# Performance work log

Hardware: AMD Instinct MI355X
Metric: run time of the kernel (lower is better)

The kernel has to match this reference:

```python
import jax, jax.numpy as jnp
import numpy as np

REALSHAPE = (32, 256, 256)   # even dims required
SHAPE = (32, 256, 129)       # rfft half-spectrum shape
MIDS = (16, 128, 128)
KCUT = 4
B, C = 4, 3


def _hs_np(f):
    # numpy mirror of Fourier.hermitian_symmetric (used only to build the constant feed mask)
    m0, m1, m2 = MIDS
    f = f.copy()
    f[m0+1:, 0, 0] = f[1:m0, 0, 0][::-1].conj()
    f[m0+1:, 0, m2] = f[1:m0, 0, m2][::-1].conj()
    f[m0+1:, m1, 0] = f[1:m0, m1, 0][::-1].conj()
    f[m0+1:, m1, m2] = f[1:m0, m1, m2][::-1].conj()
    f[0, m1+1:, 0] = f[0, 1:m1, 0][::-1].conj()
    f[0, m1+1:, m2] = f[0, 1:m1, m2][::-1].conj()
    f[m0, m1+1:, 0] = f[m0, 1:m1, 0][::-1].conj()
    f[m0, m1+1:, m2] = f[m0, 1:m1, m2][::-1].conj()
    f[m0+1:, m1+1:, 0] = f[1:m0, 1:m1, 0][::-1, ::-1].conj()
    f[m0+1:, 1:m1, 0] = f[1:m0, m1+1:, 0][::-1, ::-1].conj()
    f[m0+1:, m1+1:, m2] = f[1:m0, 1:m1, m2][::-1, ::-1].conj()
    f[m0+1:, 1:m1, m2] = f[1:m0, m1+1:, m2][::-1, ::-1].conj()
    return f


def _constants():
    ks = [np.fft.fftfreq(d, 1.0 / d) for d in SHAPE[:-1]] + [np.arange(SHAPE[-1])]
    kgrid = np.array(np.meshgrid(*ks, indexing='ij'))
    ksq = np.sum(kgrid ** 2, axis=0)
    holders = np.stack(np.meshgrid(*[np.arange(d) for d in SHAPE], indexing='ij'))
    same = np.all(np.stack([_hs_np(h) for h in holders]) == holders, axis=0)
    rem = same & (ksq <= KCUT ** 2)
    feed = np.stack([rem, rem.copy()])
    m0, m1, m2 = MIDS
    for idx in [(0, 0, 0), (0, 0, m2), (0, m1, 0), (0, m1, m2),
                (m0, 0, 0), (m0, 0, m2), (m0, m1, 0), (m0, m1, m2)]:
        feed[(1,) + idx] = False  # purely real corner modes
    feed_idx = np.nonzero(feed.reshape(-1))[0].astype(np.int32)
    ks_sel = np.stack([ksq, ksq])[feed]  # dimscale = (1,1,1)
    Pk = (1.0 / (ks_sel + 1.0) * float(np.prod(REALSHAPE))).astype(np.float32)
    grid = np.stack(np.meshgrid(*[np.arange(d) for d in REALSHAPE], indexing='ij')).astype(np.float32)
    return feed_idx, Pk, grid


def setup_inputs() -> dict:
    feed_idx, Pk, grid = _constants()
    key = jax.random.key(0)
    k1, k2 = jax.random.split(key)
    fr = jax.random.normal(k1, (B, C) + REALSHAPE, jnp.float32)
    seeds = jax.random.normal(k2, (1, 3 * feed_idx.size), jnp.float32)
    return {
        'fr': fr,
        'seeds': seeds,
        'Pk': jnp.asarray(Pk),
        'defscale': jnp.ones(3, jnp.float32),  # defscale / dimscale
        'grid': jnp.asarray(grid),
        'feed_idx': jnp.asarray(feed_idx),
    }


def _hs(f):
    # jax hermitian-symmetrize the rfft half-spectrum (writes are non-overlapping with reads)
    m0, m1, m2 = MIDS
    fl = lambda a: jnp.flip(a, 0).conj()
    fl2 = lambda a: jnp.flip(a, (0, 1)).conj()
    f = f.at[m0+1:, 0, 0].set(fl(f[1:m0, 0, 0]))
    f = f.at[m0+1:, 0, m2].set(fl(f[1:m0, 0, m2]))
    f = f.at[m0+1:, m1, 0].set(fl(f[1:m0, m1, 0]))
    f = f.at[m0+1:, m1, m2].set(fl(f[1:m0, m1, m2]))
    f = f.at[0, m1+1:, 0].set(fl(f[0, 1:m1, 0]))
    f = f.at[0, m1+1:, m2].set(fl(f[0, 1:m1, m2]))
    f = f.at[m0, m1+1:, 0].set(fl(f[m0, 1:m1, 0]))
    f = f.at[m0, m1+1:, m2].set(fl(f[m0, 1:m1, m2]))
    f = f.at[m0+1:, m1+1:, 0].set(fl2(f[1:m0, 1:m1, 0]))
    f = f.at[m0+1:, 1:m1, 0].set(fl2(f[1:m0, m1+1:, 0]))
    f = f.at[m0+1:, m1+1:, m2].set(fl2(f[1:m0, 1:m1, m2]))
    f = f.at[m0+1:, 1:m1, m2].set(fl2(f[1:m0, m1+1:, m2]))
    return f


def _forward(fr, seeds, Pk, defscale, grid, feed_idx):
    fdim = feed_idx.shape[0]
    # scale sparse coefficients by the power spectrum
    x = seeds.reshape(3, fdim) * Pk[None, :] * defscale[:, None]
    # scatter into the (2, *SHAPE) re/im spectrum via flat indices
    nfull = 2 * int(np.prod(SHAPE))
    arr = jnp.zeros((3, nfull), jnp.float32).at[:, feed_idx].set(x).reshape(3, 2, *SHAPE)
    comp = (arr[:, 0] + 1j * arr[:, 1]).astype(jnp.complex64)
    comp = jax.vmap(_hs)(comp)
    disp = jnp.fft.irfftn(comp[None], s=REALSHAPE, axes=(2, 3, 4))  # (1,3,D,H,W) float32
    D, H, W = REALSHAPE
    norm = (jnp.asarray(REALSHAPE, jnp.float32) - 1.0)[None, :, None, None, None]
    moved = 2.0 * ((grid[None] - disp) / norm) - 1.0  # normalized coords in [-1,1]
    gz, gy, gx = moved[0, 0], moved[0, 1], moved[0, 2]  # torch grid channel order [2,1,0] -> (x=W, y=H, z=D)
    # grid_sample: bilinear, padding_mode='border' (clamp float coords), align_corners=True
    fz = jnp.clip((gz + 1.0) * 0.5 * (D - 1), 0.0, D - 1)
    fy = jnp.clip((gy + 1.0) * 0.5 * (H - 1), 0.0, H - 1)
    fx = jnp.clip((gx + 1.0) * 0.5 * (W - 1), 0.0, W - 1)
    z0 = jnp.floor(fz); y0 = jnp.floor(fy); x0 = jnp.floor(fx)
    wz = fz - z0; wy = fy - y0; wx = fx - x0  # (D,H,W), broadcast against (B,C,D,H,W)
    z0i = z0.astype(jnp.int32); z1i = jnp.minimum(z0i + 1, D - 1)
    y0i = y0.astype(jnp.int32); y1i = jnp.minimum(y0i + 1, H - 1)
    x0i = x0.astype(jnp.int32); x1i = jnp.minimum(x0i + 1, W - 1)
    g = lambda zi, yi, xi: fr[:, :, zi, yi, xi]  # gather -> (B,C,D,H,W)
    c00 = g(z0i, y0i, x0i) * (1 - wx) + g(z0i, y0i, x1i) * wx
    c01 = g(z0i, y1i, x0i) * (1 - wx) + g(z0i, y1i, x1i) * wx
    c10 = g(z1i, y0i, x0i) * (1 - wx) + g(z1i, y0i, x1i) * wx
    c11 = g(z1i, y1i, x0i) * (1 - wx) + g(z1i, y1i, x1i) * wx
    c0 = c00 * (1 - wy) + c01 * wy
    c1 = c10 * (1 - wy) + c11 * wy
    return c0 * (1 - wz) + c1 * wz


def reference(fr, seeds, Pk, defscale, grid, feed_idx):
    return _forward(fr, seeds, Pk, defscale, grid, feed_idx)
```

## Files before the change

### kernel.cpp

```cpp
#include <hip/hip_runtime.h>
#include <math.h>

#define D0 32
#define D1 256
#define D2 256
#define HS2 129
#define NVOX (D0*D1*D2)
#define KMAX 4
#define NK 9
#define NK2 5
#define NCH 3
#define BATCH 4
#define FCH 3
#define NBC (BATCH*FCH)
#define C_FLOATS (NCH*NK*NK*NK2*2)

typedef float v2f __attribute__((ext_vector_type(2)));

__global__ __launch_bounds__(256) void build_S(
    const float* __restrict__ seeds, const float* __restrict__ Pk,
    const float* __restrict__ defscale, const int* __restrict__ feed_idx,
    int fdim, float* __restrict__ S)
{
    __shared__ float C[C_FLOATS];
    __shared__ int fed[NK*NK];
    int t = threadIdx.x;
    for (int i = t; i < C_FLOATS; i += 256) C[i] = 0.0f;
    if (t < NK*NK) fed[t] = 0;
    __syncthreads();
    float ds0 = defscale[0], ds1 = defscale[1], ds2 = defscale[2];
    const int STR_RI = D0 * D1 * HS2;
    const int STR_A  = D1 * HS2;
    for (int j = t; j < fdim; j += 256) {
        int idx = feed_idx[j];
        int ri = idx / STR_RI; int r = idx - ri * STR_RI;
        int a  = r / STR_A;    r -= a * STR_A;
        int b  = r / HS2;      int c = r - b * HS2;
        int k0 = (a < D0/2) ? a : a - D0;
        int k1 = (b < D1/2) ? b : b - D1;
        if (k0 < -KMAX || k0 > KMAX || k1 < -KMAX || k1 > KMAX || c > KMAX) continue;
        int i0 = k0 + KMAX, i1 = k1 + KMAX;
        float pk = Pk[j];
        int base = ((i0*NK + i1)*NK2 + c)*2 + ri;
        C[base]                 = seeds[0*fdim + j] * pk * ds0;
        C[base + 1*NK*NK*NK2*2] = seeds[1*fdim + j] * pk * ds1;
        C[base + 2*NK*NK*NK2*2] = seeds[2*fdim + j] * pk * ds2;
        if (c == 0) fed[i0*NK + i1] = 1;
    }
    __syncthreads();
    if (t < NK*NK && !fed[t]) {
        int i0 = t / NK, i1 = t - i0*NK;
        int m0 = (NK-1) - i0, m1 = (NK-1) - i1;
        for (int ch = 0; ch < NCH; ++ch) {
            int dst = ((ch*NK*NK + i0*NK + i1)*NK2 + 0)*2;
            int src = ((ch*NK*NK + m0*NK + m1)*NK2 + 0)*2;
            C[dst]   = C[src];
            C[dst+1] = -C[src+1];
        }
    }
    __syncthreads();

    int zyl = t >> 3;
    int g   = t & 7;
    int zy = blockIdx.x * 32 + zyl;
    int z = zy >> 8, y = zy & 255;

    float w0r[NK], w0i[NK], w1r[NK], w1i[NK];
    {
        float th = (float)z * (6.28318530717958647692f / (float)D0);
        float sb, cb; __sincosf(th, &sb, &cb);
        w0r[KMAX] = 1.0f; w0i[KMAX] = 0.0f;
        float pr = 1.0f, pi = 0.0f;
        #pragma unroll
        for (int k = 1; k <= KMAX; ++k) {
            float nr = pr*cb - pi*sb, ni = pr*sb + pi*cb;
            pr = nr; pi = ni;
            w0r[KMAX+k] = pr; w0i[KMAX+k] = pi;
            w0r[KMAX-k] = pr; w0i[KMAX-k] = -pi;
        }
    }
    {
        float th = (float)y * (6.28318530717958647692f / (float)D1);
        float sb, cb; __sincosf(th, &sb, &cb);
        w1r[KMAX] = 1.0f; w1i[KMAX] = 0.0f;
        float pr = 1.0f, pi = 0.0f;
        #pragma unroll
        for (int k = 1; k <= KMAX; ++k) {
            float nr = pr*cb - pi*sb, ni = pr*sb + pi*cb;
            pr = nr; pi = ni;
            w1r[KMAX+k] = pr; w1i[KMAX+k] = pi;
            w1r[KMAX-k] = pr; w1i[KMAX-k] = -pi;
        }
    }

    float Sr[NCH*NK2], Si[NCH*NK2];
    #pragma unroll
    for (int i = 0; i < NCH*NK2; ++i) { Sr[i] = 0.0f; Si[i] = 0.0f; }

    for (int m = g; m < NK*NK; m += 8) {
        int i0 = m / NK, i1 = m - i0*NK;
        float Tr = w0r[i0]*w1r[i1] - w0i[i0]*w1i[i1];
        float Ti = w0r[i0]*w1i[i1] + w0i[i0]*w1r[i1];
        const float* Cp = C + m*NK2*2;
        #pragma unroll
        for (int ch = 0; ch < NCH; ++ch) {
            #pragma unroll
            for (int k2 = 0; k2 < NK2; ++k2) {
                float cr = Cp[ch*(NK*NK*NK2*2) + k2*2];
                float ci = Cp[ch*(NK*NK*NK2*2) + k2*2 + 1];
                int o = ch*NK2 + k2;
                Sr[o] += cr*Tr - ci*Ti;
                Si[o] += cr*Ti + ci*Tr;
            }
        }
    }

    #pragma unroll
    for (int off = 4; off >= 1; off >>= 1) {
        #pragma unroll
        for (int i = 0; i < NCH*NK2; ++i) {
            Sr[i] += __shfl_down(Sr[i], off, 8);
            Si[i] += __shfl_down(Si[i], off, 8);
        }
    }

    if (g == 0) {
        const float invN = 1.0f / (float)NVOX;
        float* Sp = S + (size_t)zy * 32;
        #pragma unroll
        for (int ch = 0; ch < NCH; ++ch) {
            #pragma unroll
            for (int k2 = 0; k2 < NK2; ++k2) {
                int o = ch*NK2 + k2;
                float sc = (k2 == 0) ? invN : 2.0f*invN;
                Sp[ch*10 + k2*2 + 0] = Sr[o] * sc;
                Sp[ch*10 + k2*2 + 1] = Si[o] * sc;
            }
        }
    }
}

__global__ __launch_bounds__(256) void deform_sample(
    const float* __restrict__ fr, const float* __restrict__ S,
    float* __restrict__ out)
{
    int i = blockIdx.x;
    int u = i & 7;
    int b  = u >> 1;
    int zh = u & 1;
    int j = i >> 3;
    int z = (zh << 4) + (j >> 8);
    int y = j & 255;
    int zy = (z << 8) + y;
    int x = threadIdx.x;

    const float* __restrict__ Sp = S + (size_t)zy * 32;
    float s[30];
    #pragma unroll
    for (int q = 0; q < 30; ++q) s[q] = Sp[q];

    float th = (float)x * (6.28318530717958647692f / (float)D2);
    float sb, cb; __sincosf(th, &sb, &cb);
    float ckr[KMAX], cks[KMAX];
    ckr[0] = cb; cks[0] = sb;
    #pragma unroll
    for (int k = 1; k < KMAX; ++k) {
        float nr = ckr[k-1]*cb - cks[k-1]*sb;
        float ni = cks[k-1]*cb + ckr[k-1]*sb;
        ckr[k] = nr; cks[k] = ni;
    }

    float d[NCH];
    #pragma unroll
    for (int ch = 0; ch < NCH; ++ch) {
        float acc = s[ch*10 + 0];
        #pragma unroll
        for (int k = 1; k <= KMAX; ++k)
            acc += s[ch*10 + k*2]*ckr[k-1] - s[ch*10 + k*2 + 1]*cks[k-1];
        d[ch] = acc;
    }

    float fz = fminf(fmaxf((float)z - d[0], 0.0f), (float)(D0-1));
    float fy = fminf(fmaxf((float)y - d[1], 0.0f), (float)(D1-1));
    float fx = fminf(fmaxf((float)x - d[2], 0.0f), (float)(D2-1));

    float z0f = floorf(fz), y0f = floorf(fy), x0f = floorf(fx);
    int z0 = (int)z0f, y0 = (int)y0f, x0 = (int)x0f;
    int z1 = min(z0 + 1, D0-1), y1 = min(y0 + 1, D1-1);
    float wz = fz - z0f, wy = fy - y0f, wx = fx - x0f;

    int xm = min(x0, D2-2);
    bool hi = (x0 > xm);

    int o00 = (z0 << 16) + (y0 << 8) + xm;
    int o01 = (z0 << 16) + (y1 << 8) + xm;
    int o10 = (z1 << 16) + (y0 << 8) + xm;
    int o11 = (z1 << 16) + (y1 << 8) + xm;

    v2f P[FCH][4];
    #pragma unroll
    for (int c = 0; c < FCH; ++c) {
        const float* __restrict__ v = fr + ((size_t)(b*FCH + c) << 21);
        P[c][0] = *(const v2f*)(v + o00);
        P[c][1] = *(const v2f*)(v + o01);
        P[c][2] = *(const v2f*)(v + o10);
        P[c][3] = *(const v2f*)(v + o11);
    }

    size_t ob = ((size_t)(b*FCH) << 21) + ((size_t)zy << 8) + x;
    #pragma unroll
    for (int c = 0; c < FCH; ++c) {
        float a00 = hi ? P[c][0].y : P[c][0].x;
        float a01 = hi ? P[c][1].y : P[c][1].x;
        float a10 = hi ? P[c][2].y : P[c][2].x;
        float a11 = hi ? P[c][3].y : P[c][3].x;
        float c00 = a00 + wx * (P[c][0].y - a00);
        float c01 = a01 + wx * (P[c][1].y - a01);
        float c10 = a10 + wx * (P[c][2].y - a10);
        float c11 = a11 + wx * (P[c][3].y - a11);
        float c0 = c00 + wy * (c01 - c00);
        float c1 = c10 + wy * (c11 - c10);
        __builtin_nontemporal_store(c0 + wz * (c1 - c0),
                                    &out[ob + ((size_t)c << 21)]);
    }
}

extern "C" void kernel_launch(void* const* d_in, const int* in_sizes, int n_in,
                              void* d_out, int out_size, void* d_ws, size_t ws_size,
                              hipStream_t stream) {
    const float* fr       = (const float*)d_in[0];
    const float* seeds    = (const float*)d_in[1];
    const float* Pk       = (const float*)d_in[2];
    const float* defscale = (const float*)d_in[3];
    const int*   feed_idx = (const int*)d_in[5];
    int fdim = in_sizes[2];

    float* S = (float*)d_ws;

    build_S<<<256, 256, 0, stream>>>(seeds, Pk, defscale, feed_idx, fdim, S);
    deform_sample<<<8192*4, 256, 0, stream>>>(fr, S, (float*)d_out);
}
```

Measured before the change: 281.4 us.

## Add L3 prefetch kernel and process two rows per thread in deform_sample

Adds a warm_l3 kernel that streams all of fr with float4 loads so the input sits in the last-level cache before the gather kernel runs. deform_sample now handles two adjacent y rows per thread, issuing all 24 gather loads up front behind a sched_barrier to raise memory-level parallelism, and it halves the grid. Output stores change from nontemporal to regular stores. The warm-up pass adds a full extra read of fr (about 100 MB) and the two-row version uses more registers.

```diff
diff --git a/kernel.cpp b/kernel.cpp
--- a/kernel.cpp
+++ b/kernel.cpp
@@ -16,6 +16,21 @@
 #define C_FLOATS (NCH*NK*NK*NK2*2)
 
 typedef float v2f __attribute__((ext_vector_type(2)));
+
+
+__global__ __launch_bounds__(256) void warm_l3(
+    const float4* __restrict__ fr4)
+{
+    int tid = blockIdx.x * 256 + threadIdx.x;
+    const int stride = 2048 * 256;
+    float ax = 0.f, ay = 0.f, az = 0.f, aw = 0.f;
+    #pragma unroll
+    for (int k = 0; k < 12; ++k) {
+        float4 v = fr4[tid + k * stride];
+        ax += v.x; ay += v.y; az += v.z; aw += v.w;
+    }
+    asm volatile("" :: "v"(ax), "v"(ay), "v"(az), "v"(aw));
+}
 
 __global__ __launch_bounds__(256) void build_S(
     const float* __restrict__ seeds, const float* __restrict__ Pk,
@@ -149,15 +164,18 @@
     int b  = u >> 1;
     int zh = u & 1;
     int j = i >> 3;
-    int z = (zh << 4) + (j >> 8);
-    int y = j & 255;
-    int zy = (z << 8) + y;
+    int z = (zh << 4) + (j >> 7);
+    int yA = (j & 127) << 1;
+    int yB = yA + 1;
+    int zyA = (z << 8) + yA;
     int x = threadIdx.x;
 
-    const float* __restrict__ Sp = S + (size_t)zy * 32;
-    float s[30];
-    #pragma unroll
-    for (int q = 0; q < 30; ++q) s[q] = Sp[q];
+    const float* __restrict__ Sp = S + (size_t)zyA * 32;
+    float sA[30], sB[30];
+    #pragma unroll
+    for (int q = 0; q < 30; ++q) sA[q] = Sp[q];
+    #pragma unroll
+    for (int q = 0; q < 30; ++q) sB[q] = Sp[32 + q];
 
     float th = (float)x * (6.28318530717958647692f / (float)D2);
     float sb, cb; __sincosf(th, &sb, &cb);
@@ -170,58 +188,98 @@
         ckr[k] = nr; cks[k] = ni;
     }
 
-    float d[NCH];
+    float dA[NCH], dB[NCH];
     #pragma unroll
     for (int ch = 0; ch < NCH; ++ch) {
-        float acc = s[ch*10 + 0];
-        #pragma unroll
-        for (int k = 1; k <= KMAX; ++k)
-            acc += s[ch*10 + k*2]*ckr[k-1] - s[ch*10 + k*2 + 1]*cks[k-1];
-        d[ch] = acc;
-    }
-
-    float fz = fminf(fmaxf((float)z - d[0], 0.0f), (float)(D0-1));
-    float fy = fminf(fmaxf((float)y - d[1], 0.0f), (float)(D1-1));
-    float fx = fminf(fmaxf((float)x - d[2], 0.0f), (float)(D2-1));
-
-    float z0f = floorf(fz), y0f = floorf(fy), x0f = floorf(fx);
-    int z0 = (int)z0f, y0 = (int)y0f, x0 = (int)x0f;
-    int z1 = min(z0 + 1, D0-1), y1 = min(y0 + 1, D1-1);
-    float wz = fz - z0f, wy = fy - y0f, wx = fx - x0f;
-
-    int xm = min(x0, D2-2);
-    bool hi = (x0 > xm);
-
-    int o00 = (z0 << 16) + (y0 << 8) + xm;
-    int o01 = (z0 << 16) + (y1 << 8) + xm;
-    int o10 = (z1 << 16) + (y0 << 8) + xm;
-    int o11 = (z1 << 16) + (y1 << 8) + xm;
-
-    v2f P[FCH][4];
+        float aA = sA[ch*10 + 0];
+        float aB = sB[ch*10 + 0];
+        #pragma unroll
+        for (int k = 1; k <= KMAX; ++k) {
+            aA += sA[ch*10 + k*2]*ckr[k-1] - sA[ch*10 + k*2 + 1]*cks[k-1];
+            aB += sB[ch*10 + k*2]*ckr[k-1] - sB[ch*10 + k*2 + 1]*cks[k-1];
+        }
+        dA[ch] = aA; dB[ch] = aB;
+    }
+
+    float fzA = fminf(fmaxf((float)z  - dA[0], 0.0f), (float)(D0-1));
+    float fyA = fminf(fmaxf((float)yA - dA[1], 0.0f), (float)(D1-1));
+    float fxA = fminf(fmaxf((float)x  - dA[2], 0.0f), (float)(D2-1));
+    float z0fA = floorf(fzA), y0fA = floorf(fyA), x0fA = floorf(fxA);
+    int z0A = (int)z0fA, y0A = (int)y0fA, x0A = (int)x0fA;
+    int z1A = min(z0A + 1, D0-1), y1A = min(y0A + 1, D1-1);
+    float wzA = fzA - z0fA, wyA = fyA - y0fA, wxA = fxA - x0fA;
+    int xmA = min(x0A, D2-2);
+    bool hiA = (x0A > xmA);
+    int o00A = (z0A << 16) + (y0A << 8) + xmA;
+    int o01A = (z0A << 16) + (y1A << 8) + xmA;
+    int o10A = (z1A << 16) + (y0A << 8) + xmA;
+    int o11A = (z1A << 16) + (y1A << 8) + xmA;
+
+    float fzB = fminf(fmaxf((float)z  - dB[0], 0.0f), (float)(D0-1));
+    float fyB = fminf(fmaxf((float)yB - dB[1], 0.0f), (float)(D1-1));
+    float fxB = fminf(fmaxf((float)x  - dB[2], 0.0f), (float)(D2-1));
+    float z0fB = floorf(fzB), y0fB = floorf(fyB), x0fB = floorf(fxB);
+    int z0B = (int)z0fB, y0B = (int)y0fB, x0B = (int)x0fB;
+    int z1B = min(z0B + 1, D0-1), y1B = min(y0B + 1, D1-1);
+    float wzB = fzB - z0fB, wyB = fyB - y0fB, wxB = fxB - x0fB;
+    int xmB = min(x0B, D2-2);
+    bool hiB = (x0B > xmB);
+    int o00B = (z0B << 16) + (y0B << 8) + xmB;
+    int o01B = (z0B << 16) + (y1B << 8) + xmB;
+    int o10B = (z1B << 16) + (y0B << 8) + xmB;
+    int o11B = (z1B << 16) + (y1B << 8) + xmB;
+
+    const float* __restrict__ vb = fr + ((size_t)(b*FCH) << 21);
+    v2f PA[FCH][4], PB[FCH][4];
     #pragma unroll
     for (int c = 0; c < FCH; ++c) {
-        const float* __restrict__ v = fr + ((size_t)(b*FCH + c) << 21);
-        P[c][0] = *(const v2f*)(v + o00);
-        P[c][1] = *(const v2f*)(v + o01);
-        P[c][2] = *(const v2f*)(v + o10);
-        P[c][3] = *(const v2f*)(v + o11);
-    }
-
-    size_t ob = ((size_t)(b*FCH) << 21) + ((size_t)zy << 8) + x;
+        const float* __restrict__ v = vb + ((size_t)c << 21);
+        PA[c][0] = *(const v2f*)(v + o00A);
+        PA[c][1] = *(const v2f*)(v + o01A);
+        PA[c][2] = *(const v2f*)(v + o10A);
+        PA[c][3] = *(const v2f*)(v + o11A);
+    }
     #pragma unroll
     for (int c = 0; c < FCH; ++c) {
-        float a00 = hi ? P[c][0].y : P[c][0].x;
-        float a01 = hi ? P[c][1].y : P[c][1].x;
-        float a10 = hi ? P[c][2].y : P[c][2].x;
-        float a11 = hi ? P[c][3].y : P[c][3].x;
-        float c00 = a00 + wx * (P[c][0].y - a00);
-        float c01 = a01 + wx * (P[c][1].y - a01);
-        float c10 = a10 + wx * (P[c][2].y - a10);
-        float c11 = a11 + wx * (P[c][3].y - a11);
-        float c0 = c00 + wy * (c01 - c00);
-        float c1 = c10 + wy * (c11 - c10);
-        __builtin_nontemporal_store(c0 + wz * (c1 - c0),
-                                    &out[ob + ((size_t)c << 21)]);
+        const float* __restrict__ v = vb + ((size_t)c << 21);
+        PB[c][0] = *(const v2f*)(v + o00B);
+        PB[c][1] = *(const v2f*)(v + o01B);
+        PB[c][2] = *(const v2f*)(v + o10B);
+        PB[c][3] = *(const v2f*)(v + o11B);
+    }
+    __builtin_amdgcn_sched_barrier(0);
+
+    size_t ob = ((size_t)(b*FCH) << 21) + ((size_t)zyA << 8) + x;
+
+    #pragma unroll
+    for (int c = 0; c < FCH; ++c) {
+        float a00 = hiA ? PA[c][0].y : PA[c][0].x;
+        float a01 = hiA ? PA[c][1].y : PA[c][1].x;
+        float a10 = hiA ? PA[c][2].y : PA[c][2].x;
+        float a11 = hiA ? PA[c][3].y : PA[c][3].x;
+        float c00 = a00 + wxA * (PA[c][0].y - a00);
+        float c01 = a01 + wxA * (PA[c][1].y - a01);
+        float c10 = a10 + wxA * (PA[c][2].y - a10);
+        float c11 = a11 + wxA * (PA[c][3].y - a11);
+        float c0 = c00 + wyA * (c01 - c00);
+        float c1 = c10 + wyA * (c11 - c10);
+        out[ob + ((size_t)c << 21)] = c0 + wzA * (c1 - c0);
+    }
+    __builtin_amdgcn_sched_barrier(0);
+
+    #pragma unroll
+    for (int c = 0; c < FCH; ++c) {
+        float a00 = hiB ? PB[c][0].y : PB[c][0].x;
+        float a01 = hiB ? PB[c][1].y : PB[c][1].x;
+        float a10 = hiB ? PB[c][2].y : PB[c][2].x;
+        float a11 = hiB ? PB[c][3].y : PB[c][3].x;
+        float c00 = a00 + wxB * (PB[c][0].y - a00);
+        float c01 = a01 + wxB * (PB[c][1].y - a01);
+        float c10 = a10 + wxB * (PB[c][2].y - a10);
+        float c11 = a11 + wxB * (PB[c][3].y - a11);
+        float c0 = c00 + wyB * (c01 - c00);
+        float c1 = c10 + wyB * (c11 - c10);
+        out[ob + 256 + ((size_t)c << 21)] = c0 + wzB * (c1 - c0);
     }
 }
 
@@ -237,6 +295,7 @@
 
     float* S = (float*)d_ws;
 
+    warm_l3<<<2048, 256, 0, stream>>>((const float4*)fr);
     build_S<<<256, 256, 0, stream>>>(seeds, Pk, defscale, feed_idx, fdim, S);
-    deform_sample<<<8192*4, 256, 0, stream>>>(fr, S, (float*)d_out);
+    deform_sample<<<16384, 256, 0, stream>>>(fr, S, (float*)d_out);
 }
```

Result: faster. 271.8 us (-3.4%).
